# Kernel optimization log

Measured on AMD Instinct MI355X. Metric: run time of the kernel, lower is better.

The kernel has to match this reference:

```python
import jax, jax.numpy as jnp
import numpy as np

TEMPERATURE = 0.07
NUM_UNIFY_CLASSES = 256


def setup_inputs() -> dict:
    key = jax.random.key(0)
    k1, k2, k3 = jax.random.split(key, 3)
    b, c, h, w = 16, 256, 128, 128
    # small-magnitude feats so exp(logits) stays finite at temperature 0.07
    feats = jax.random.normal(k1, (b, c, h, w), dtype=jnp.float32) * 0.05
    queue = jax.random.normal(k2, (NUM_UNIFY_CLASSES, c), dtype=jnp.float32)
    queue = queue / jnp.linalg.norm(queue, axis=1, keepdims=True)  # unit rows, as a memory bank would hold
    labels = jax.random.randint(k3, (b * h * w, NUM_UNIFY_CLASSES), 0, 2, dtype=jnp.int32)
    return {"feats": feats, "queue": queue, "labels": labels}


def reference(feats, queue, labels):
    b, c, h, w = feats.shape
    # [b,c,h,w] -> [N, c]
    f = jnp.transpose(feats, (0, 2, 3, 1)).reshape(-1, c)
    # [N, M] logits
    logits = (f @ queue.T) / TEMPERATURE
    pos_mask = labels.reshape(-1, NUM_UNIFY_CLASSES).astype(logits.dtype)
    neg_mask = 1.0 - pos_mask
    sum_neg = jnp.sum(jnp.exp(logits) * neg_mask, axis=1)   # [N]
    sum_pos = jnp.sum(jnp.exp(-logits) * pos_mask, axis=1)  # [N]
    loss = jnp.log(sum_neg * sum_pos + 1.0)                 # [N]
    lb_num = jnp.sum(loss != 0)
    return jnp.where(lb_num == 0, jnp.float32(0.0),
                     jnp.sum(loss) / jnp.maximum(lb_num, 1).astype(loss.dtype))
```

## Files before the change

kernel.cpp:

```cpp
#include <hip/hip_runtime.h>
#include <hip/hip_bf16.h>


typedef __bf16 bf16x8 __attribute__((ext_vector_type(8)));
typedef float floatx4 __attribute__((ext_vector_type(4)));

__device__ __forceinline__ unsigned int pack_bf2(float a, float b) {
  unsigned int ua = __float_as_uint(a) + 0x8000u;
  unsigned int ub = __float_as_uint(b) + 0x8000u;
  return (ua >> 16) | (ub & 0xffff0000u);
}

__global__ void qprep(const float* __restrict__ queue,
                      unsigned short* __restrict__ qs,
                      float* __restrict__ accum) {
  const int gt = blockIdx.x * 256 + threadIdx.x;
  const int t = gt >> 6;
  const int lane = gt & 63;
  const int m = ((t >> 3) << 4) | (lane & 15);
  const int k0 = ((t & 7) << 5) | ((lane >> 4) << 3);
  const float* qr = queue + m * 256 + k0;
  const float TINV = 14.2857142857142857f;
  union { unsigned int u32[4]; uint4 v; } u;
#pragma unroll
  for (int j = 0; j < 4; ++j)
    u.u32[j] = pack_bf2(qr[2 * j] * TINV, qr[2 * j + 1] * TINV);
  *(uint4*)(qs + (size_t)gt * 8) = u.v;
  if (gt == 0) { accum[0] = 0.0f; accum[1] = 0.0f; }
}

__global__ __launch_bounds__(256, 3) void pcl_main(
    const float* __restrict__ feats,
    const int* __restrict__ labels,
    const unsigned short* __restrict__ qs,
    float* __restrict__ accum) {
  __shared__ uint4 Bs[2048];
  __shared__ float Red[8][64];

  const int bx = blockIdx.x;
  const int bidx = bx >> 8;
  const int hw0 = (bx & 255) << 6;
  const int tid = threadIdx.x;
  const int w = tid >> 6;
  const int lane = tid & 63;
  const int qd = lane >> 4;
  const int s = lane & 15;

  const float* gb = feats + (size_t)bidx * 4194304 + (size_t)hw0 + lane;
  float f[64];
#pragma unroll
  for (int i = 0; i < 64; ++i)
    f[i] = gb[(size_t)((w << 6) + i) * 16384];

  const size_t nbase = (size_t)bx << 6;
  const int cbase = (w << 6) | (qd << 2);
  int4 labv[16];
#pragma unroll
  for (int mt = 0; mt < 4; ++mt)
#pragma unroll
    for (int nt = 0; nt < 4; ++nt)
      labv[(mt << 2) + nt] =
          *(const int4*)(labels + ((nbase + (nt << 4) + s) << 8) + cbase + (mt << 4));

#pragma unroll
  for (int g = 0; g < 8; ++g) {
    uint4 u;
    u.x = pack_bf2(f[8 * g + 0], f[8 * g + 1]);
    u.y = pack_bf2(f[8 * g + 2], f[8 * g + 3]);
    u.z = pack_bf2(f[8 * g + 4], f[8 * g + 5]);
    u.w = pack_bf2(f[8 * g + 6], f[8 * g + 7]);
    const int kg = (w << 3) + g;
    Bs[(((kg >> 2) << 2) + qd) * 64 + ((kg & 3) << 4) + s] = u;
  }

  unsigned int m0 = 0, m1 = 0;
#pragma unroll
  for (int mt = 0; mt < 4; ++mt) {
#pragma unroll
    for (int nt = 0; nt < 4; ++nt) {
      const int4 lb = labv[(mt << 2) + nt];
      const unsigned int b = ((mt & 1) << 4) | (nt << 2);
      unsigned int bits = ((lb.x != 0) ? 1u : 0u) | ((lb.y != 0) ? 2u : 0u) |
                          ((lb.z != 0) ? 4u : 0u) | ((lb.w != 0) ? 8u : 0u);
      if (mt < 2) m0 |= bits << b; else m1 |= bits << b;
    }
  }

  floatx4 acc[4][4];
#pragma unroll
  for (int mt = 0; mt < 4; ++mt)
#pragma unroll
    for (int nt = 0; nt < 4; ++nt)
      acc[mt][nt] = floatx4{0.0f, 0.0f, 0.0f, 0.0f};

  __syncthreads();

  const bf16x8* qfrag = (const bf16x8*)qs;
  const bf16x8* Bf = (const bf16x8*)Bs;
#pragma unroll
  for (int ks = 0; ks < 8; ++ks) {
    bf16x8 af[4];
#pragma unroll
    for (int mt = 0; mt < 4; ++mt)
      af[mt] = qfrag[(((((w << 2) + mt) << 3) | ks) << 6) + lane];
    bf16x8 bfv[4];
#pragma unroll
    for (int nt = 0; nt < 4; ++nt)
      bfv[nt] = Bf[(((ks << 2) + nt) << 6) + lane];
#pragma unroll
    for (int mt = 0; mt < 4; ++mt)
#pragma unroll
      for (int nt = 0; nt < 4; ++nt)
        acc[mt][nt] = __builtin_amdgcn_mfma_f32_16x16x32_bf16(af[mt], bfv[nt],
                                                              acc[mt][nt], 0, 0, 0);
  }

  float nn[4] = {0.f, 0.f, 0.f, 0.f};
  float pp[4] = {0.f, 0.f, 0.f, 0.f};
#pragma unroll
  for (int mt = 0; mt < 4; ++mt) {
    const unsigned int mm = (mt < 2) ? m0 : m1;
#pragma unroll
    for (int nt = 0; nt < 4; ++nt) {
      const floatx4 a = acc[mt][nt];
      const unsigned int base = ((mt & 1) << 4) | (nt << 2);
#pragma unroll
      for (int c = 0; c < 4; ++c) {
        const unsigned int p = (mm >> (base + c)) & 1u;
        const float ls = __uint_as_float(__float_as_uint(a[c]) ^ (p << 31));
        const float e = __expf(ls);
        nn[nt] += p ? 0.0f : e;
        pp[nt] += p ? e : 0.0f;
      }
    }
  }

#pragma unroll
  for (int nt = 0; nt < 4; ++nt) {
    nn[nt] += __shfl_xor(nn[nt], 16);
    nn[nt] += __shfl_xor(nn[nt], 32);
    pp[nt] += __shfl_xor(pp[nt], 16);
    pp[nt] += __shfl_xor(pp[nt], 32);
  }
  if (lane < 16) {
#pragma unroll
    for (int nt = 0; nt < 4; ++nt) {
      Red[(w << 1) | 0][(nt << 4) + lane] = nn[nt];
      Red[(w << 1) | 1][(nt << 4) + lane] = pp[nt];
    }
  }
  __syncthreads();

  if (tid < 64) {
    const float sn = Red[0][tid] + Red[2][tid] + Red[4][tid] + Red[6][tid];
    const float sp = Red[1][tid] + Red[3][tid] + Red[5][tid] + Red[7][tid];
    float loss = logf(sn * sp + 1.0f);
    float c = (loss != 0.0f) ? 1.0f : 0.0f;
#pragma unroll
    for (int off = 32; off > 0; off >>= 1) {
      loss += __shfl_xor(loss, off);
      c += __shfl_xor(c, off);
    }
    if (tid == 0) {
      atomicAdd(&accum[0], loss);
      atomicAdd(&accum[1], c);
    }
  }
}

__global__ void pcl_finalize(const float* __restrict__ accum,
                             float* __restrict__ out) {
  const float ssum = accum[0];
  const float c = accum[1];
  out[0] = (c != 0.0f) ? (ssum / c) : 0.0f;
}

extern "C" void kernel_launch(void* const* d_in, const int* in_sizes, int n_in,
                              void* d_out, int out_size, void* d_ws, size_t ws_size,
                              hipStream_t stream) {
  (void)in_sizes; (void)n_in; (void)out_size; (void)ws_size;
  const float* feats = (const float*)d_in[0];
  const float* queue = (const float*)d_in[1];
  const int* labels = (const int*)d_in[2];

  unsigned short* qs = (unsigned short*)d_ws;
  float* accum = (float*)((char*)d_ws + 256 * 256 * sizeof(unsigned short));

  qprep<<<32, 256, 0, stream>>>(queue, qs, accum);
  pcl_main<<<4096, 256, 0, stream>>>(feats, labels, qs, accum);
  pcl_finalize<<<1, 1, 0, stream>>>(accum, (float*)d_out);
}
```

Baseline: 566.4 us.

## Precompute label bitmasks and double-buffer feature tiles in persistent blocks

Adds a separate kernel that compresses the int32 label matrix into per-pixel bitmasks in a transposed layout. The main kernel then runs 512-thread blocks that each loop over four 64-pixel tiles, prefetching the next tile's features and mask words while the MFMAs for the current tile run from double-buffered shared memory. The goal is to hide global load latency and shrink the label traffic seen by the GEMM kernel. The cost is an extra kernel pass that still reads all 268 MB of labels and writes a mask buffer, plus more block-level syncs per tile.

```diff
diff --git a/kernel.cpp b/kernel.cpp
--- a/kernel.cpp
+++ b/kernel.cpp
@@ -4,6 +4,8 @@
 
 typedef __bf16 bf16x8 __attribute__((ext_vector_type(8)));
 typedef float floatx4 __attribute__((ext_vector_type(4)));
+
+#define N_PIX 262144
 
 __device__ __forceinline__ unsigned int pack_bf2(float a, float b) {
   unsigned int ua = __float_as_uint(a) + 0x8000u;
@@ -29,143 +31,184 @@
   if (gt == 0) { accum[0] = 0.0f; accum[1] = 0.0f; }
 }
 
-__global__ __launch_bounds__(256, 3) void pcl_main(
+__global__ __launch_bounds__(256) void lcomp(const int* __restrict__ labels,
+                                             unsigned* __restrict__ maskT) {
+  const int tid = threadIdx.x;
+  const int lane = tid & 63;
+  const int wave = (blockIdx.x << 2) + (tid >> 6);
+  const int p0 = wave << 6;
+  const int* lb = labels + ((size_t)p0 << 8) + (lane << 2);
+  const int sh = (lane & 7) << 2;
+  const bool writer = (lane & 7) == 0;
+  unsigned* wp = maskT + ((size_t)(lane >> 3) * N_PIX) + p0;
+
+#pragma unroll
+  for (int c8 = 0; c8 < 8; ++c8) {
+    int4 lv[8];
+#pragma unroll
+    for (int i = 0; i < 8; ++i)
+      lv[i] = *(const int4*)(lb + (((c8 << 3) + i) << 8));
+#pragma unroll
+    for (int i = 0; i < 8; ++i) {
+      unsigned v = ((lv[i].x != 0) ? 1u : 0u) | ((lv[i].y != 0) ? 2u : 0u) |
+                   ((lv[i].z != 0) ? 4u : 0u) | ((lv[i].w != 0) ? 8u : 0u);
+      v <<= sh;
+      v |= __shfl_xor(v, 1);
+      v |= __shfl_xor(v, 2);
+      v |= __shfl_xor(v, 4);
+      if (writer) wp[(c8 << 3) + i] = v;
+    }
+  }
+}
+
+__global__ __launch_bounds__(512, 4) void pcl_main(
     const float* __restrict__ feats,
-    const int* __restrict__ labels,
+    const unsigned* __restrict__ maskT,
     const unsigned short* __restrict__ qs,
     float* __restrict__ accum) {
-  __shared__ uint4 Bs[2048];
-  __shared__ float Red[8][64];
-
-  const int bx = blockIdx.x;
-  const int bidx = bx >> 8;
-  const int hw0 = (bx & 255) << 6;
+  __shared__ uint4 Bs[2][2048];
+  __shared__ float Red[16][64];
+
   const int tid = threadIdx.x;
   const int w = tid >> 6;
   const int lane = tid & 63;
   const int qd = lane >> 4;
   const int s = lane & 15;
-
-  const float* gb = feats + (size_t)bidx * 4194304 + (size_t)hw0 + lane;
-  float f[64];
-#pragma unroll
-  for (int i = 0; i < 64; ++i)
-    f[i] = gb[(size_t)((w << 6) + i) * 16384];
-
-  const size_t nbase = (size_t)bx << 6;
-  const int cbase = (w << 6) | (qd << 2);
-  int4 labv[16];
-#pragma unroll
-  for (int mt = 0; mt < 4; ++mt)
-#pragma unroll
-    for (int nt = 0; nt < 4; ++nt)
-      labv[(mt << 2) + nt] =
-          *(const int4*)(labels + ((nbase + (nt << 4) + s) << 8) + cbase + (mt << 4));
-
-#pragma unroll
-  for (int g = 0; g < 8; ++g) {
-    uint4 u;
-    u.x = pack_bf2(f[8 * g + 0], f[8 * g + 1]);
-    u.y = pack_bf2(f[8 * g + 2], f[8 * g + 3]);
-    u.z = pack_bf2(f[8 * g + 4], f[8 * g + 5]);
-    u.w = pack_bf2(f[8 * g + 6], f[8 * g + 7]);
-    const int kg = (w << 3) + g;
-    Bs[(((kg >> 2) << 2) + qd) * 64 + ((kg & 3) << 4) + s] = u;
+  const int T0 = blockIdx.x << 2;
+
+  const bf16x8* qfrag = (const bf16x8*)qs;
+  const int chB = (w << 5) + ((lane >> 4) << 3);
+  const int px4 = (lane & 15) << 2;
+  const int kg = (w << 2) + (lane >> 4);
+  const unsigned* mp = maskT + (size_t)w * N_PIX;
+
+  floatx4 frv[8];
+  unsigned mk[2][4];
+  float lacc = 0.0f, cacc = 0.0f;
+
+#define ISSUE_TILE(T, MB)                                                     \
+  do {                                                                        \
+    const float* fb = feats + ((size_t)((T) >> 8) << 22) + (((T) & 255) << 6);\
+    _Pragma("unroll") for (int j = 0; j < 8; ++j)                             \
+        frv[j] = *(const floatx4*)(fb + (size_t)(chB + j) * 16384 + px4);     \
+    _Pragma("unroll") for (int nt = 0; nt < 4; ++nt)                          \
+        mk[MB][nt] = mp[((T) << 6) + (nt << 4) + s];                          \
+  } while (0)
+
+#define PACK_TILE(BUF)                                                        \
+  do {                                                                        \
+    _Pragma("unroll") for (int jj = 0; jj < 4; ++jj) {                        \
+      const int n = px4 + jj;                                                 \
+      uint4 u;                                                                \
+      u.x = pack_bf2(frv[0][jj], frv[1][jj]);                                 \
+      u.y = pack_bf2(frv[2][jj], frv[3][jj]);                                 \
+      u.z = pack_bf2(frv[4][jj], frv[5][jj]);                                 \
+      u.w = pack_bf2(frv[6][jj], frv[7][jj]);                                 \
+      Bs[BUF][(((kg >> 2) << 2) + (n >> 4)) * 64 + ((kg & 3) << 4) + (n & 15)] = u; \
+    }                                                                         \
+  } while (0)
+
+  ISSUE_TILE(T0, 0);
+  PACK_TILE(0);
+  __syncthreads();
+
+  for (int t = 0; t < 4; ++t) {
+    const int cur = t & 1;
+    if (t < 3) ISSUE_TILE(T0 + t + 1, 1 - cur);
+
+    floatx4 acc[2][4];
+#pragma unroll
+    for (int mt = 0; mt < 2; ++mt)
+#pragma unroll
+      for (int nt = 0; nt < 4; ++nt)
+        acc[mt][nt] = floatx4{0.0f, 0.0f, 0.0f, 0.0f};
+
+    const bf16x8* Bf = (const bf16x8*)Bs[cur];
+#pragma unroll
+    for (int mt = 0; mt < 2; ++mt) {
+      const int m16 = (w << 1) + mt;
+#pragma unroll
+      for (int kh = 0; kh < 2; ++kh) {
+        bf16x8 af[4];
+#pragma unroll
+        for (int kk = 0; kk < 4; ++kk)
+          af[kk] = qfrag[(((m16 << 3) + (kh << 2) + kk) << 6) + lane];
+#pragma unroll
+        for (int kk = 0; kk < 4; ++kk) {
+          const int ks = (kh << 2) + kk;
+#pragma unroll
+          for (int nt = 0; nt < 4; ++nt) {
+            const bf16x8 bv = Bf[(((ks << 2) + nt) << 6) + lane];
+            acc[mt][nt] = __builtin_amdgcn_mfma_f32_16x16x32_bf16(
+                af[kk], bv, acc[mt][nt], 0, 0, 0);
+          }
+        }
+      }
+    }
+
+    float nn[4] = {0.f, 0.f, 0.f, 0.f};
+    float pp[4] = {0.f, 0.f, 0.f, 0.f};
+#pragma unroll
+    for (int mt = 0; mt < 2; ++mt) {
+#pragma unroll
+      for (int nt = 0; nt < 4; ++nt) {
+        const floatx4 a = acc[mt][nt];
+        const unsigned mw = mk[cur][nt];
+#pragma unroll
+        for (int r = 0; r < 4; ++r) {
+          const unsigned p = (mw >> ((mt << 4) + (qd << 2) + r)) & 1u;
+          const float ls = __uint_as_float(__float_as_uint(a[r]) ^ (p << 31));
+          const float e = __expf(ls);
+          nn[nt] += p ? 0.0f : e;
+          pp[nt] += p ? e : 0.0f;
+        }
+      }
+    }
+#pragma unroll
+    for (int nt = 0; nt < 4; ++nt) {
+      nn[nt] += __shfl_xor(nn[nt], 16);
+      nn[nt] += __shfl_xor(nn[nt], 32);
+      pp[nt] += __shfl_xor(pp[nt], 16);
+      pp[nt] += __shfl_xor(pp[nt], 32);
+    }
+    if (lane < 16) {
+#pragma unroll
+      for (int nt = 0; nt < 4; ++nt) {
+        Red[(w << 1) | 0][(nt << 4) + lane] = nn[nt];
+        Red[(w << 1) | 1][(nt << 4) + lane] = pp[nt];
+      }
+    }
+    __syncthreads();
+
+    if (tid < 64) {
+      float sn = 0.f, sp = 0.f;
+#pragma unroll
+      for (int ww = 0; ww < 8; ++ww) {
+        sn += Red[(ww << 1) | 0][tid];
+        sp += Red[(ww << 1) | 1][tid];
+      }
+      const float loss = logf(sn * sp + 1.0f);
+      lacc += loss;
+      cacc += (loss != 0.0f) ? 1.0f : 0.0f;
+    }
+
+    if (t < 3) PACK_TILE(1 - cur);
+    __syncthreads();
   }
 
-  unsigned int m0 = 0, m1 = 0;
-#pragma unroll
-  for (int mt = 0; mt < 4; ++mt) {
-#pragma unroll
-    for (int nt = 0; nt < 4; ++nt) {
-      const int4 lb = labv[(mt << 2) + nt];
-      const unsigned int b = ((mt & 1) << 4) | (nt << 2);
-      unsigned int bits = ((lb.x != 0) ? 1u : 0u) | ((lb.y != 0) ? 2u : 0u) |
-                          ((lb.z != 0) ? 4u : 0u) | ((lb.w != 0) ? 8u : 0u);
-      if (mt < 2) m0 |= bits << b; else m1 |= bits << b;
+  if (tid < 64) {
+#pragma unroll
+    for (int off = 32; off > 0; off >>= 1) {
+      lacc += __shfl_xor(lacc, off);
+      cacc += __shfl_xor(cacc, off);
+    }
+    if (tid == 0) {
+      atomicAdd(&accum[0], lacc);
+      atomicAdd(&accum[1], cacc);
     }
   }
-
-  floatx4 acc[4][4];
-#pragma unroll
-  for (int mt = 0; mt < 4; ++mt)
-#pragma unroll
-    for (int nt = 0; nt < 4; ++nt)
-      acc[mt][nt] = floatx4{0.0f, 0.0f, 0.0f, 0.0f};
-
-  __syncthreads();
-
-  const bf16x8* qfrag = (const bf16x8*)qs;
-  const bf16x8* Bf = (const bf16x8*)Bs;
-#pragma unroll
-  for (int ks = 0; ks < 8; ++ks) {
-    bf16x8 af[4];
-#pragma unroll
-    for (int mt = 0; mt < 4; ++mt)
-      af[mt] = qfrag[(((((w << 2) + mt) << 3) | ks) << 6) + lane];
-    bf16x8 bfv[4];
-#pragma unroll
-    for (int nt = 0; nt < 4; ++nt)
-      bfv[nt] = Bf[(((ks << 2) + nt) << 6) + lane];
-#pragma unroll
-    for (int mt = 0; mt < 4; ++mt)
-#pragma unroll
-      for (int nt = 0; nt < 4; ++nt)
-        acc[mt][nt] = __builtin_amdgcn_mfma_f32_16x16x32_bf16(af[mt], bfv[nt],
-                                                              acc[mt][nt], 0, 0, 0);
-  }
-
-  float nn[4] = {0.f, 0.f, 0.f, 0.f};
-  float pp[4] = {0.f, 0.f, 0.f, 0.f};
-#pragma unroll
-  for (int mt = 0; mt < 4; ++mt) {
-    const unsigned int mm = (mt < 2) ? m0 : m1;
-#pragma unroll
-    for (int nt = 0; nt < 4; ++nt) {
-      const floatx4 a = acc[mt][nt];
-      const unsigned int base = ((mt & 1) << 4) | (nt << 2);
-#pragma unroll
-      for (int c = 0; c < 4; ++c) {
-        const unsigned int p = (mm >> (base + c)) & 1u;
-        const float ls = __uint_as_float(__float_as_uint(a[c]) ^ (p << 31));
-        const float e = __expf(ls);
-        nn[nt] += p ? 0.0f : e;
-        pp[nt] += p ? e : 0.0f;
-      }
-    }
-  }
-
-#pragma unroll
-  for (int nt = 0; nt < 4; ++nt) {
-    nn[nt] += __shfl_xor(nn[nt], 16);
-    nn[nt] += __shfl_xor(nn[nt], 32);
-    pp[nt] += __shfl_xor(pp[nt], 16);
-    pp[nt] += __shfl_xor(pp[nt], 32);
-  }
-  if (lane < 16) {
-#pragma unroll
-    for (int nt = 0; nt < 4; ++nt) {
-      Red[(w << 1) | 0][(nt << 4) + lane] = nn[nt];
-      Red[(w << 1) | 1][(nt << 4) + lane] = pp[nt];
-    }
-  }
-  __syncthreads();
-
-  if (tid < 64) {
-    const float sn = Red[0][tid] + Red[2][tid] + Red[4][tid] + Red[6][tid];
-    const float sp = Red[1][tid] + Red[3][tid] + Red[5][tid] + Red[7][tid];
-    float loss = logf(sn * sp + 1.0f);
-    float c = (loss != 0.0f) ? 1.0f : 0.0f;
-#pragma unroll
-    for (int off = 32; off > 0; off >>= 1) {
-      loss += __shfl_xor(loss, off);
-      c += __shfl_xor(c, off);
-    }
-    if (tid == 0) {
-      atomicAdd(&accum[0], loss);
-      atomicAdd(&accum[1], c);
-    }
-  }
+#undef ISSUE_TILE
+#undef PACK_TILE
 }
 
 __global__ void pcl_finalize(const float* __restrict__ accum,
@@ -183,10 +226,12 @@
   const float* queue = (const float*)d_in[1];
   const int* labels = (const int*)d_in[2];
 
-  unsigned short* qs = (unsigned short*)d_ws;
-  float* accum = (float*)((char*)d_ws + 256 * 256 * sizeof(unsigned short));
-
+  unsigned* maskT = (unsigned*)d_ws;
+  unsigned short* qs = (unsigned short*)((char*)d_ws + (size_t)8 * N_PIX * 4);
+  float* accum = (float*)((char*)qs + 256 * 256 * sizeof(unsigned short));
+
+  lcomp<<<1024, 256, 0, stream>>>(labels, maskT);
   qprep<<<32, 256, 0, stream>>>(queue, qs, accum);
-  pcl_main<<<4096, 256, 0, stream>>>(feats, labels, qs, accum);
+  pcl_main<<<1024, 512, 0, stream>>>(feats, maskT, qs, accum);
   pcl_finalize<<<1, 1, 0, stream>>>(accum, (float*)d_out);
 }
```

Measured after the change: 576.8 us. Within noise of the previous version (+1.8%).

## Split feature and label preprocessing into separate streaming kernels

Applied to the files above, without the earlier changes.

Adds an fprep kernel that converts feats to bf16 MFMA-ready tiles in workspace and an lcomp kernel that packs labels into per-pixel bitmasks. The main kernel then loads the prepared tiles directly into LDS via global_load_lds and reads compact masks, freeing registers and raising the occupancy hint. This reduces per-thread register pressure and strided loads in the main kernel, at the cost of an extra round-trip of bf16 feature tiles through global memory and two more launches.

```diff
diff --git a/kernel.cpp b/kernel.cpp
--- a/kernel.cpp
+++ b/kernel.cpp
@@ -4,6 +4,11 @@
 
 typedef __bf16 bf16x8 __attribute__((ext_vector_type(8)));
 typedef float floatx4 __attribute__((ext_vector_type(4)));
+
+using gl_void = const __attribute__((address_space(1))) void;
+using lds_void = __attribute__((address_space(3))) void;
+
+#define N_PIX 262144
 
 __device__ __forceinline__ unsigned int pack_bf2(float a, float b) {
   unsigned int ua = __float_as_uint(a) + 0x8000u;
@@ -29,62 +34,95 @@
   if (gt == 0) { accum[0] = 0.0f; accum[1] = 0.0f; }
 }
 
-__global__ __launch_bounds__(256, 3) void pcl_main(
-    const float* __restrict__ feats,
-    const int* __restrict__ labels,
+__global__ __launch_bounds__(256) void fprep(const float* __restrict__ feats,
+                                             uint4* __restrict__ ptiles) {
+  const int b = blockIdx.x;
+  const int T = b >> 3;
+  const int cg = b & 7;
+  const int w = threadIdx.x >> 6;
+  const int lane = threadIdx.x & 63;
+  const int kg = (cg << 2) + w;
+  const int batch = T >> 8;
+  const int pix0 = (T & 255) << 6;
+
+  const float* gp = feats + ((size_t)batch << 22) + ((size_t)(kg << 3) << 14) +
+                    pix0 + lane;
+  float f[8];
+#pragma unroll
+  for (int j = 0; j < 8; ++j) f[j] = gp[(size_t)j << 14];
+
+  uint4 u;
+  u.x = pack_bf2(f[0], f[1]);
+  u.y = pack_bf2(f[2], f[3]);
+  u.z = pack_bf2(f[4], f[5]);
+  u.w = pack_bf2(f[6], f[7]);
+  ptiles[(size_t)T * 2048 +
+         ((((kg >> 2) << 2) + (lane >> 4)) << 6) + ((kg & 3) << 4) + (lane & 15)] = u;
+}
+
+__global__ __launch_bounds__(256) void lcomp(const int* __restrict__ labels,
+                                             unsigned* __restrict__ maskT) {
+  const int tid = threadIdx.x;
+  const int lane = tid & 63;
+  const int wave = (blockIdx.x << 2) + (tid >> 6);
+  const int p0 = wave << 6;
+  const int* lb = labels + ((size_t)p0 << 8) + (lane << 2);
+  const int sh = (lane & 7) << 2;
+  const bool writer = (lane & 7) == 0;
+  unsigned* wp = maskT + ((size_t)(lane >> 3) * N_PIX) + p0;
+
+#pragma unroll
+  for (int c8 = 0; c8 < 8; ++c8) {
+    int4 lv[8];
+#pragma unroll
+    for (int i = 0; i < 8; ++i)
+      lv[i] = *(const int4*)(lb + (((c8 << 3) + i) << 8));
+#pragma unroll
+    for (int i = 0; i < 8; ++i) {
+      unsigned v = ((lv[i].x != 0) ? 1u : 0u) | ((lv[i].y != 0) ? 2u : 0u) |
+                   ((lv[i].z != 0) ? 4u : 0u) | ((lv[i].w != 0) ? 8u : 0u);
+      v <<= sh;
+      v |= __shfl_xor(v, 1);
+      v |= __shfl_xor(v, 2);
+      v |= __shfl_xor(v, 4);
+      if (writer) wp[(c8 << 3) + i] = v;
+    }
+  }
+}
+
+__global__ __launch_bounds__(256, 4) void pcl_main(
+    const uint4* __restrict__ ptiles,
+    const unsigned* __restrict__ maskT,
     const unsigned short* __restrict__ qs,
     float* __restrict__ accum) {
   __shared__ uint4 Bs[2048];
   __shared__ float Red[8][64];
 
-  const int bx = blockIdx.x;
-  const int bidx = bx >> 8;
-  const int hw0 = (bx & 255) << 6;
+  const int T = blockIdx.x;
   const int tid = threadIdx.x;
   const int w = tid >> 6;
   const int lane = tid & 63;
   const int qd = lane >> 4;
   const int s = lane & 15;
-
-  const float* gb = feats + (size_t)bidx * 4194304 + (size_t)hw0 + lane;
-  float f[64];
-#pragma unroll
-  for (int i = 0; i < 64; ++i)
-    f[i] = gb[(size_t)((w << 6) + i) * 16384];
-
-  const size_t nbase = (size_t)bx << 6;
-  const int cbase = (w << 6) | (qd << 2);
-  int4 labv[16];
-#pragma unroll
-  for (int mt = 0; mt < 4; ++mt)
+  const int pix0 = T << 6;
+
+  {
+    const char* gsrc = (const char*)(ptiles + (size_t)T * 2048) +
+                       ((w << 3) << 10) + (lane << 4);
+#pragma unroll
+    for (int i = 0; i < 8; ++i) {
+      uint4* lp = &Bs[((w << 3) + i) << 6];
+      __builtin_amdgcn_global_load_lds((gl_void*)(gsrc + (i << 10)),
+                                       (lds_void*)lp, 16, 0, 0);
+    }
+  }
+
+  unsigned mk[2][4];
+#pragma unroll
+  for (int j = 0; j < 2; ++j)
 #pragma unroll
     for (int nt = 0; nt < 4; ++nt)
-      labv[(mt << 2) + nt] =
-          *(const int4*)(labels + ((nbase + (nt << 4) + s) << 8) + cbase + (mt << 4));
-
-#pragma unroll
-  for (int g = 0; g < 8; ++g) {
-    uint4 u;
-    u.x = pack_bf2(f[8 * g + 0], f[8 * g + 1]);
-    u.y = pack_bf2(f[8 * g + 2], f[8 * g + 3]);
-    u.z = pack_bf2(f[8 * g + 4], f[8 * g + 5]);
-    u.w = pack_bf2(f[8 * g + 6], f[8 * g + 7]);
-    const int kg = (w << 3) + g;
-    Bs[(((kg >> 2) << 2) + qd) * 64 + ((kg & 3) << 4) + s] = u;
-  }
-
-  unsigned int m0 = 0, m1 = 0;
-#pragma unroll
-  for (int mt = 0; mt < 4; ++mt) {
-#pragma unroll
-    for (int nt = 0; nt < 4; ++nt) {
-      const int4 lb = labv[(mt << 2) + nt];
-      const unsigned int b = ((mt & 1) << 4) | (nt << 2);
-      unsigned int bits = ((lb.x != 0) ? 1u : 0u) | ((lb.y != 0) ? 2u : 0u) |
-                          ((lb.z != 0) ? 4u : 0u) | ((lb.w != 0) ? 8u : 0u);
-      if (mt < 2) m0 |= bits << b; else m1 |= bits << b;
-    }
-  }
+      mk[j][nt] = maskT[(size_t)((w << 1) + j) * N_PIX + pix0 + (nt << 4) + s];
 
   floatx4 acc[4][4];
 #pragma unroll
@@ -119,15 +157,15 @@
   float pp[4] = {0.f, 0.f, 0.f, 0.f};
 #pragma unroll
   for (int mt = 0; mt < 4; ++mt) {
-    const unsigned int mm = (mt < 2) ? m0 : m1;
 #pragma unroll
     for (int nt = 0; nt < 4; ++nt) {
       const floatx4 a = acc[mt][nt];
-      const unsigned int base = ((mt & 1) << 4) | (nt << 2);
-#pragma unroll
-      for (int c = 0; c < 4; ++c) {
-        const unsigned int p = (mm >> (base + c)) & 1u;
-        const float ls = __uint_as_float(__float_as_uint(a[c]) ^ (p << 31));
+      const unsigned mw = mk[mt >> 1][nt];
+      const unsigned base = ((mt & 1) << 4) | (qd << 2);
+#pragma unroll
+      for (int r = 0; r < 4; ++r) {
+        const unsigned p = (mw >> (base + r)) & 1u;
+        const float ls = __uint_as_float(__float_as_uint(a[r]) ^ (p << 31));
         const float e = __expf(ls);
         nn[nt] += p ? 0.0f : e;
         pp[nt] += p ? e : 0.0f;
@@ -183,10 +221,14 @@
   const float* queue = (const float*)d_in[1];
   const int* labels = (const int*)d_in[2];
 
-  unsigned short* qs = (unsigned short*)d_ws;
-  float* accum = (float*)((char*)d_ws + 256 * 256 * sizeof(unsigned short));
+  uint4* ptiles = (uint4*)d_ws;
+  unsigned* maskT = (unsigned*)((char*)d_ws + ((size_t)4096 * 32768));
+  unsigned short* qs = (unsigned short*)((char*)maskT + (size_t)8 * N_PIX * 4);
+  float* accum = (float*)((char*)qs + 256 * 256 * sizeof(unsigned short));
 
   qprep<<<32, 256, 0, stream>>>(queue, qs, accum);
-  pcl_main<<<4096, 256, 0, stream>>>(feats, labels, qs, accum);
+  fprep<<<32768, 256, 0, stream>>>(feats, ptiles);
+  lcomp<<<1024, 256, 0, stream>>>(labels, maskT);
+  pcl_main<<<4096, 256, 0, stream>>>(ptiles, maskT, qs, accum);
   pcl_finalize<<<1, 1, 0, stream>>>(accum, (float*)d_out);
 }
```

After: 662.9 us. 1.17x slower.
